# Performance work log

Measured on AMD Instinct MI355X. Metric: run time of the kernel, lower is better.

## Reference

```python
import jax, jax.numpy as jnp
import numpy as np

GRID_RANGE = ((-3.0, 3.0), (-3.0, 3.0))
GRID_SHAPE = (64, 64)
INIT_LENGTHSCALE = 0.1


def _construct_grid():
    axes = [jnp.linspace(lo, hi, s, dtype=jnp.float32)
            for (lo, hi), s in zip(GRID_RANGE, GRID_SHAPE)]
    mesh = jnp.meshgrid(*axes, indexing='ij')
    return jnp.stack(mesh, axis=-1)  # [64, 64, dx]


def setup_inputs() -> dict:
    key = jax.random.key(0)
    k1, k2 = jax.random.split(key)
    m, n, dx, dz = 8, 4096, 2, 16
    x = jax.random.normal(k1, (m, n, dx), dtype=jnp.float32)
    z = jax.random.normal(k2, (m, n, dz), dtype=jnp.float32)
    # lengthscale_param = log(exp(init_lengthscale) - 1), per dim
    ls_param = jnp.log(jnp.expm1(jnp.full((dx,), INIT_LENGTHSCALE, dtype=jnp.float32)))
    grid = _construct_grid()
    return {"x": x, "z": z, "lengthscale_param": ls_param, "grid": grid}


def reference(x, z, lengthscale_param, grid):
    # lengthscale = 1e-5 + softplus(param), per input dim
    ls = 1e-5 + jax.nn.softplus(lengthscale_param)  # [dx]
    m = x.shape[0]
    grid_flat = grid.reshape(-1, grid.shape[-1])  # [M, dx]
    # per-dim scaled differences; sum((g-x)^2 / ls^2) == sum(((g-x)/ls)^2)
    diff = (grid_flat[None, :, None, :] - x[:, None, :, :]) / ls  # [m, M, n, dx]
    pre_exp = jnp.sum(diff * diff, axis=-1)                        # [m, M, n]
    weights = jnp.exp(-0.5 * pre_exp)                              # [m, M, n]
    z_grid_flat = jnp.einsum('bmn,bnd->bmd', weights, z)           # [m, M, dz]
    z_grid = z_grid_flat.reshape((m,) + grid.shape[:-1] + (z.shape[-1],))
    x_grid = jnp.broadcast_to(grid[None], (m,) + grid.shape)
    return (x_grid, z_grid)
```

## Files before the change

### kernel.cpp

```cpp
#include <hip/hip_runtime.h>
#include <hip/hip_bf16.h>
#include <cstdint>

#define N_PTS   4096
#define M_GRID  4096
#define SKIP_E0 -20.0f

typedef __attribute__((ext_vector_type(8))) short  short8;
typedef __attribute__((ext_vector_type(4))) float  floatx4;

#define OFF_LIST 0
#define OFF_XS   16384
#define OFF_ZF   49152
#define OFF_RED  49152
#define OFF_CNT  57344
#define SMEM_BYTES 57348

__global__ __launch_bounds__(512, 4)
void setconv_kernel(const float2* __restrict__ x2,
                    const float4* __restrict__ z4,
                    const float*  __restrict__ lsp,
                    const float2* __restrict__ grid2,
                    float2*       __restrict__ outx,
                    float*        __restrict__ outz)
{
    __shared__ __align__(16) char smem[SMEM_BYTES];
    int*            list = reinterpret_cast<int*>(smem + OFF_LIST);
    float2*         xs   = reinterpret_cast<float2*>(smem + OFF_XS);
    __hip_bfloat16* zf   = reinterpret_cast<__hip_bfloat16*>(smem + OFF_ZF);
    floatx4*        redv = reinterpret_cast<floatx4*>(smem + OFF_RED);
    int*            cntp = reinterpret_cast<int*>(smem + OFF_CNT);

    const int tid  = threadIdx.x;
    const int lane = tid & 63;
    const int w    = tid >> 6;
    const int mt   = w & 3;
    const int ks   = w >> 2;
    const int gtile = blockIdx.x;
    const int b     = blockIdx.y;

    float p0 = lsp[0], p1 = lsp[1];
    float sp0 = (p0 > 0.f) ? (p0 + log1pf(expf(-p0))) : log1pf(expf(p0));
    float sp1 = (p1 > 0.f) ? (p1 + log1pf(expf(-p1))) : log1pf(expf(p1));
    float ls0 = 1e-5f + sp0, ls1 = 1e-5f + sp1;
    const float q0 = -0.5f / (ls0 * ls0);
    const float q1 = -0.5f / (ls1 * ls1);

    const float2 gv = grid2[gtile * 64 + lane];
    const float  g0 = gv.x;
    if (w == 0) outx[(size_t)b * M_GRID + gtile * 64 + lane] = gv;
    const float g1m = grid2[gtile * 64 + mt * 16 + (lane & 15)].y;

    if (tid == 0) *cntp = 0;
    __syncthreads();

    const float2* xb  = x2 + b * N_PTS;
    const float2* zb2 = reinterpret_cast<const float2*>(z4 + (size_t)b * N_PTS * 4);

    for (int t = tid; t < N_PTS; t += 512) {
        float2 xv = xb[t];
        float d0 = g0 - xv.x;
        float e0 = q0 * d0 * d0;
        bool keep = (e0 >= SKIP_E0);
        unsigned long long m = __ballot(keep);
        int base = 0;
        if (lane == 0 && m) base = atomicAdd(cntp, __popcll(m));
        base = __shfl(base, 0);
        if (keep) {
            int off = __popcll(m & ((1ull << lane) - 1ull));
            list[base + off] = t;
            xs[base + off]   = make_float2(e0, xv.y);
        }
    }
    __syncthreads();
    const int C    = *cntp;
    const int Cpad = (C + 63) & ~63;
    for (int t = C + tid; t < Cpad; t += 512) {
        list[t] = 0;
        xs[t]   = make_float2(-1e30f, 0.f);
    }
    __syncthreads();

    const int ngroup = Cpad >> 6;

    auto stage = [&](int gi, int bufi) {
        int row = tid >> 3;
        int p   = tid & 7;
        int n   = list[gi * 64 + row];
        float2 zz = zb2[(size_t)n * 8 + p];
        int sg = row >> 5, k = row & 31;
        int base = bufi * 2048 + sg * 1024 + (k & 7);
        int L0 = ((k >> 3) << 4) | (2 * p);
        zf[base + L0 * 8]       = __float2bfloat16(zz.x);
        zf[base + (L0 + 1) * 8] = __float2bfloat16(zz.y);
    };

    floatx4 acc = {0.f, 0.f, 0.f, 0.f};

    if (ngroup > 0) stage(0, 0);
    __syncthreads();

    for (int gi = 0; gi < ngroup; ++gi) {
        const int cur = gi & 1;
        if (gi + 1 < ngroup) stage(gi + 1, cur ^ 1);

        short8 bfrag = *reinterpret_cast<const short8*>(
            smem + OFF_ZF + cur * 4096 + ks * 2048 + lane * 16);

        const int k0 = gi * 64 + ks * 32 + (lane >> 4) * 8;
        union { uint32_t u[4]; short8 s; } af;
#pragma unroll
        for (int jp = 0; jp < 4; ++jp) {
            float2 s0 = xs[k0 + 2 * jp];
            float2 s1 = xs[k0 + 2 * jp + 1];
            float u0 = g1m - s0.y;
            float u1 = g1m - s1.y;
            float w0 = __expf(fmaf(q1 * u0, u0, s0.x));
            float w1 = __expf(fmaf(q1 * u1, u1, s1.x));
            union { __hip_bfloat162 h; uint32_t u; } cc;
            cc.h = __float22bfloat162_rn(make_float2(w0, w1));
            af.u[jp] = cc.u;
        }

        acc = __builtin_amdgcn_mfma_f32_16x16x32_bf16(af.s, bfrag, acc, 0, 0, 0);
        __syncthreads();
    }

    if (w >= 4) redv[(w - 4) * 64 + lane] = acc;
    __syncthreads();
    if (w < 4) {
        floatx4 o = redv[mt * 64 + lane];
        acc += o;
        const int n = lane & 15;
        size_t base = ((size_t)b * M_GRID + gtile * 64 + mt * 16 +
                       (lane >> 4) * 4) * 16 + n;
#pragma unroll
        for (int r = 0; r < 4; ++r)
            outz[base + (size_t)r * 16] = acc[r];
    }
}

extern "C" void kernel_launch(void* const* d_in, const int* in_sizes, int n_in,
                              void* d_out, int out_size, void* d_ws, size_t ws_size,
                              hipStream_t stream) {
    const float2* x2    = (const float2*)d_in[0];
    const float4* z4    = (const float4*)d_in[1];
    const float*  lsp   = (const float*)d_in[2];
    const float2* grid2 = (const float2*)d_in[3];
    float* out = (float*)d_out;

    hipLaunchKernelGGL(setconv_kernel, dim3(64, 8), dim3(512), 0, stream,
                       x2, z4, lsp, grid2, (float2*)out, out + 65536);
}
```

Measured before the change: 88.61 us.

## Gather z directly into MFMA B fragments and pack candidate records compactly

Drops the shared-memory staging of z tiles and the per-group barriers. Each lane now gathers its eight z values straight from global memory into the B fragment. Candidate records are packed as an 8-byte struct (e0 bits plus bf16 x1 and a 16-bit index), which shrinks LDS from about 57KB to 32KB and should raise occupancy. The cost is that x1 is stored at bf16 precision and z is gathered with scattered, uncoalesced 4-byte loads that depend on L2 and cache hits.

```diff
diff --git a/kernel.cpp b/kernel.cpp
--- a/kernel.cpp
+++ b/kernel.cpp
@@ -9,33 +9,40 @@
 typedef __attribute__((ext_vector_type(8))) short  short8;
 typedef __attribute__((ext_vector_type(4))) float  floatx4;
 
-#define OFF_LIST 0
-#define OFF_XS   16384
-#define OFF_ZF   49152
-#define OFF_RED  49152
-#define OFF_CNT  57344
-#define SMEM_BYTES 57348
+#define SMEM_BYTES 32772
+
+__device__ __forceinline__ float bits_hi_f(uint32_t u) {
+    union { uint32_t u; float f; } c; c.u = u & 0xffff0000u; return c.f;
+}
+__device__ __forceinline__ float bits_f(uint32_t u) {
+    union { uint32_t u; float f; } c; c.u = u; return c.f;
+}
+__device__ __forceinline__ uint32_t pack_bf2(float a, float b) {
+    union { __hip_bfloat162 h; uint32_t u; } c;
+    c.h = __float22bfloat162_rn(make_float2(a, b));
+    return c.u;
+}
 
 __global__ __launch_bounds__(512, 4)
 void setconv_kernel(const float2* __restrict__ x2,
-                    const float4* __restrict__ z4,
+                    const float*  __restrict__ zf,
                     const float*  __restrict__ lsp,
                     const float2* __restrict__ grid2,
                     float2*       __restrict__ outx,
                     float*        __restrict__ outz)
 {
     __shared__ __align__(16) char smem[SMEM_BYTES];
-    int*            list = reinterpret_cast<int*>(smem + OFF_LIST);
-    float2*         xs   = reinterpret_cast<float2*>(smem + OFF_XS);
-    __hip_bfloat16* zf   = reinterpret_cast<__hip_bfloat16*>(smem + OFF_ZF);
-    floatx4*        redv = reinterpret_cast<floatx4*>(smem + OFF_RED);
-    int*            cntp = reinterpret_cast<int*>(smem + OFF_CNT);
+    uint2*   rec  = reinterpret_cast<uint2*>(smem);
+    floatx4* redv = reinterpret_cast<floatx4*>(smem);
+    int*     cntp = reinterpret_cast<int*>(smem + 32768);
 
     const int tid  = threadIdx.x;
     const int lane = tid & 63;
     const int w    = tid >> 6;
     const int mt   = w & 3;
     const int ks   = w >> 2;
+    const int q    = lane >> 4;
+    const int dn   = lane & 15;
     const int gtile = blockIdx.x;
     const int b     = blockIdx.y;
 
@@ -49,13 +56,12 @@
     const float2 gv = grid2[gtile * 64 + lane];
     const float  g0 = gv.x;
     if (w == 0) outx[(size_t)b * M_GRID + gtile * 64 + lane] = gv;
-    const float g1m = grid2[gtile * 64 + mt * 16 + (lane & 15)].y;
+    const float g1m = grid2[gtile * 64 + mt * 16 + dn].y;
 
     if (tid == 0) *cntp = 0;
     __syncthreads();
 
-    const float2* xb  = x2 + b * N_PTS;
-    const float2* zb2 = reinterpret_cast<const float2*>(z4 + (size_t)b * N_PTS * 4);
+    const float2* xb = x2 + b * N_PTS;
 
     for (int t = tid; t < N_PTS; t += 512) {
         float2 xv = xb[t];
@@ -68,72 +74,69 @@
         base = __shfl(base, 0);
         if (keep) {
             int off = __popcll(m & ((1ull << lane) - 1ull));
-            list[base + off] = t;
-            xs[base + off]   = make_float2(e0, xv.y);
+            __hip_bfloat16 hx = __float2bfloat16(xv.y);
+            uint32_t x1n = ((uint32_t)*reinterpret_cast<uint16_t*>(&hx) << 16)
+                         | (uint32_t)t;
+            union { float f; uint32_t u; } ee; ee.f = e0;
+            rec[base + off] = make_uint2(ee.u, x1n);
         }
     }
     __syncthreads();
     const int C    = *cntp;
     const int Cpad = (C + 63) & ~63;
     for (int t = C + tid; t < Cpad; t += 512) {
-        list[t] = 0;
-        xs[t]   = make_float2(-1e30f, 0.f);
+        union { float f; uint32_t u; } ee; ee.f = -1e30f;
+        rec[t] = make_uint2(ee.u, 0u);
     }
     __syncthreads();
 
     const int ngroup = Cpad >> 6;
-
-    auto stage = [&](int gi, int bufi) {
-        int row = tid >> 3;
-        int p   = tid & 7;
-        int n   = list[gi * 64 + row];
-        float2 zz = zb2[(size_t)n * 8 + p];
-        int sg = row >> 5, k = row & 31;
-        int base = bufi * 2048 + sg * 1024 + (k & 7);
-        int L0 = ((k >> 3) << 4) | (2 * p);
-        zf[base + L0 * 8]       = __float2bfloat16(zz.x);
-        zf[base + (L0 + 1) * 8] = __float2bfloat16(zz.y);
-    };
+    const float* zcol = zf + (size_t)b * (N_PTS * 16) + dn;
 
     floatx4 acc = {0.f, 0.f, 0.f, 0.f};
 
-    if (ngroup > 0) stage(0, 0);
-    __syncthreads();
+    for (int gi = 0; gi < ngroup; ++gi) {
+        const int k0 = (gi << 6) + (ks << 5) + (q << 3);
+        const uint4* rq = reinterpret_cast<const uint4*>(rec + k0);
+        uint4 r0 = rq[0], r1 = rq[1], r2 = rq[2], r3 = rq[3];
 
-    for (int gi = 0; gi < ngroup; ++gi) {
-        const int cur = gi & 1;
-        if (gi + 1 < ngroup) stage(gi + 1, cur ^ 1);
+        float z0 = zcol[(size_t)(r0.y & 0xffffu) * 16];
+        float z1 = zcol[(size_t)(r0.w & 0xffffu) * 16];
+        float z2 = zcol[(size_t)(r1.y & 0xffffu) * 16];
+        float z3 = zcol[(size_t)(r1.w & 0xffffu) * 16];
+        float z4 = zcol[(size_t)(r2.y & 0xffffu) * 16];
+        float z5 = zcol[(size_t)(r2.w & 0xffffu) * 16];
+        float z6 = zcol[(size_t)(r3.y & 0xffffu) * 16];
+        float z7 = zcol[(size_t)(r3.w & 0xffffu) * 16];
 
-        short8 bfrag = *reinterpret_cast<const short8*>(
-            smem + OFF_ZF + cur * 4096 + ks * 2048 + lane * 16);
+        float u0 = g1m - bits_hi_f(r0.y), u1 = g1m - bits_hi_f(r0.w);
+        float u2 = g1m - bits_hi_f(r1.y), u3 = g1m - bits_hi_f(r1.w);
+        float u4 = g1m - bits_hi_f(r2.y), u5 = g1m - bits_hi_f(r2.w);
+        float u6 = g1m - bits_hi_f(r3.y), u7 = g1m - bits_hi_f(r3.w);
+        float w0 = __expf(fmaf(q1 * u0, u0, bits_f(r0.x)));
+        float w1 = __expf(fmaf(q1 * u1, u1, bits_f(r0.z)));
+        float w2 = __expf(fmaf(q1 * u2, u2, bits_f(r1.x)));
+        float w3 = __expf(fmaf(q1 * u3, u3, bits_f(r1.z)));
+        float w4 = __expf(fmaf(q1 * u4, u4, bits_f(r2.x)));
+        float w5 = __expf(fmaf(q1 * u5, u5, bits_f(r2.z)));
+        float w6 = __expf(fmaf(q1 * u6, u6, bits_f(r3.x)));
+        float w7 = __expf(fmaf(q1 * u7, u7, bits_f(r3.z)));
 
-        const int k0 = gi * 64 + ks * 32 + (lane >> 4) * 8;
-        union { uint32_t u[4]; short8 s; } af;
-#pragma unroll
-        for (int jp = 0; jp < 4; ++jp) {
-            float2 s0 = xs[k0 + 2 * jp];
-            float2 s1 = xs[k0 + 2 * jp + 1];
-            float u0 = g1m - s0.y;
-            float u1 = g1m - s1.y;
-            float w0 = __expf(fmaf(q1 * u0, u0, s0.x));
-            float w1 = __expf(fmaf(q1 * u1, u1, s1.x));
-            union { __hip_bfloat162 h; uint32_t u; } cc;
-            cc.h = __float22bfloat162_rn(make_float2(w0, w1));
-            af.u[jp] = cc.u;
-        }
+        union { uint32_t u[4]; short8 s; } af, bf;
+        af.u[0] = pack_bf2(w0, w1); af.u[1] = pack_bf2(w2, w3);
+        af.u[2] = pack_bf2(w4, w5); af.u[3] = pack_bf2(w6, w7);
+        bf.u[0] = pack_bf2(z0, z1); bf.u[1] = pack_bf2(z2, z3);
+        bf.u[2] = pack_bf2(z4, z5); bf.u[3] = pack_bf2(z6, z7);
 
-        acc = __builtin_amdgcn_mfma_f32_16x16x32_bf16(af.s, bfrag, acc, 0, 0, 0);
-        __syncthreads();
+        acc = __builtin_amdgcn_mfma_f32_16x16x32_bf16(af.s, bf.s, acc, 0, 0, 0);
     }
 
+    __syncthreads();
     if (w >= 4) redv[(w - 4) * 64 + lane] = acc;
     __syncthreads();
     if (w < 4) {
-        floatx4 o = redv[mt * 64 + lane];
-        acc += o;
-        const int n = lane & 15;
-        size_t base = ((size_t)b * M_GRID + gtile * 64 + mt * 16 +
-                       (lane >> 4) * 4) * 16 + n;
+        acc += redv[mt * 64 + lane];
+        size_t base = ((size_t)b * M_GRID + gtile * 64 + mt * 16 + q * 4) * 16 + dn;
 #pragma unroll
         for (int r = 0; r < 4; ++r)
             outz[base + (size_t)r * 16] = acc[r];
@@ -144,11 +147,11 @@
                               void* d_out, int out_size, void* d_ws, size_t ws_size,
                               hipStream_t stream) {
     const float2* x2    = (const float2*)d_in[0];
-    const float4* z4    = (const float4*)d_in[1];
+    const float*  zf    = (const float*)d_in[1];
     const float*  lsp   = (const float*)d_in[2];
     const float2* grid2 = (const float2*)d_in[3];
     float* out = (float*)d_out;
 
     hipLaunchKernelGGL(setconv_kernel, dim3(64, 8), dim3(512), 0, stream,
-                       x2, z4, lsp, grid2, (float2*)out, out + 65536);
+                       x2, zf, lsp, grid2, (float2*)out, out + 65536);
 }
```

Result: no change. 90.00 us (+1.6%).
